# Kernel optimization log

Hardware: AMD Instinct MI355X
Metric: run time of the kernel (lower is better)

## Reference

```python
import jax, jax.numpy as jnp
import numpy as np

EPS_FREE = True  # original uses plain division by norm, no epsilon


def _gram_schmidt_batched(xf):
    """xf: [B, n_experts, dim] -> orthonormal rows per sample, [B, n_experts, dim].
    Unrolled loop over n_experts (small, fixed); fully vectorized over B."""
    n = xf.shape[1]
    v0 = xf[:, 0]
    v0 = v0 / jnp.linalg.norm(v0, axis=-1, keepdims=True)
    basis = [v0]
    for i in range(1, n):
        v = xf[:, i]
        B = jnp.stack(basis, axis=1)                      # [B, i, dim]
        coeffs = jnp.einsum('bid,bd->bi', B, v)           # projections onto basis
        v = v - jnp.einsum('bi,bid->bd', coeffs, B)
        v = v / jnp.linalg.norm(v, axis=-1, keepdims=True)
        basis.append(v)
    return jnp.stack(basis, axis=1)


def setup_inputs() -> dict:
    key = jax.random.key(0)
    n_experts, n_task, batch_size, dim = 8, 8, 1024, 512
    x = jax.random.normal(key, (n_experts, n_task, batch_size, dim), dtype=jnp.float32)
    return {"x": x}


def reference(x):
    # x: [n_experts, n_task, batch_size, dim]
    x_t = x.transpose(1, 2, 0, 3)                         # [n_task, bs, n_experts, dim]
    n_task, bs, n_experts, dim = x_t.shape
    x_flat = x_t.reshape((n_task * bs, n_experts, dim))
    orth = _gram_schmidt_batched(x_flat)
    # faithful to source: output stays in [n_task, bs, n_experts, dim] layout
    return orth.reshape((n_task, bs, n_experts, dim))
```

## Files before the change

### kernel.cpp

```cpp
#include <hip/hip_runtime.h>


#define NE 8
#define DIM 512
#define NSAMP 8192

__device__ __forceinline__ float wave_sum(float p) {
#pragma unroll
    for (int off = 32; off > 0; off >>= 1)
        p += __shfl_xor(p, off, 64);
    return p;
}

__global__ __launch_bounds__(256) void gs_kernel(const float* __restrict__ x,
                                                 float* __restrict__ out) {
    const int lane = threadIdx.x & 63;
    const int w = blockIdx.x * 4 + (threadIdx.x >> 6);
    const int t = w >> 10;
    const int b = w & 1023;

    float v[NE][8];
#pragma unroll
    for (int e = 0; e < NE; ++e) {
        const float* src = x + ((size_t)(e * 8 + t) * 1024 + b) * DIM;
#pragma unroll
        for (int c = 0; c < 2; ++c) {
            float4 f = *reinterpret_cast<const float4*>(src + c * 256 + lane * 4);
            v[e][c * 4 + 0] = f.x;
            v[e][c * 4 + 1] = f.y;
            v[e][c * 4 + 2] = f.z;
            v[e][c * 4 + 3] = f.w;
        }
    }

#pragma unroll
    for (int i = 0; i < NE; ++i) {
        float coef[NE];
#pragma unroll
        for (int j = 0; j < NE; ++j) {
            if (j < i) {
                float p = 0.f;
#pragma unroll
                for (int k = 0; k < 8; ++k) p = fmaf(v[j][k], v[i][k], p);
                coef[j] = wave_sum(p);
            }
        }
#pragma unroll
        for (int k = 0; k < 8; ++k) {
            float acc = 0.f;
#pragma unroll
            for (int j = 0; j < NE; ++j) {
                if (j < i) acc = fmaf(coef[j], v[j][k], acc);
            }
            v[i][k] -= acc;
        }
        float p = 0.f;
#pragma unroll
        for (int k = 0; k < 8; ++k) p = fmaf(v[i][k], v[i][k], p);
        float nrm2 = wave_sum(p);
        float inv = 1.0f / sqrtf(nrm2);
#pragma unroll
        for (int k = 0; k < 8; ++k) v[i][k] *= inv;
    }

#pragma unroll
    for (int e = 0; e < NE; ++e) {
        float* dst = out + ((size_t)w * NE + e) * DIM;
#pragma unroll
        for (int c = 0; c < 2; ++c) {
            float4 f;
            f.x = v[e][c * 4 + 0];
            f.y = v[e][c * 4 + 1];
            f.z = v[e][c * 4 + 2];
            f.w = v[e][c * 4 + 3];
            *reinterpret_cast<float4*>(dst + c * 256 + lane * 4) = f;
        }
    }
}

extern "C" void kernel_launch(void* const* d_in, const int* in_sizes, int n_in,
                              void* d_out, int out_size, void* d_ws, size_t ws_size,
                              hipStream_t stream) {
    const float* x = (const float*)d_in[0];
    float* out = (float*)d_out;
    gs_kernel<<<NSAMP / 4, 256, 0, stream>>>(x, out);
}
```

Measured before the change: 46.79 us.

## Replace sequential Gram-Schmidt with Gram matrix plus Cholesky orthogonalization

Computes all 36 pairwise dot products of the 8 expert vectors up front and reduces them in one batched cross-lane shuffle pass, replacing 36 serialized wave reductions. It then runs a small Cholesky factorization in registers and applies forward substitution to build the orthonormal rows. This shortens the dependency chain of the reductions but is numerically less stable than classical Gram-Schmidt, and it raises register pressure. Output stores are also switched to nontemporal stores.

Measured after the change: 49.59 us. 1.06x slower.

```diff
diff --git a/kernel.cpp b/kernel.cpp
--- a/kernel.cpp
+++ b/kernel.cpp
@@ -5,15 +5,10 @@
 #define DIM 512
 #define NSAMP 8192
 
-__device__ __forceinline__ float wave_sum(float p) {
-#pragma unroll
-    for (int off = 32; off > 0; off >>= 1)
-        p += __shfl_xor(p, off, 64);
-    return p;
-}
+typedef float f32x4 __attribute__((ext_vector_type(4)));
 
-__global__ __launch_bounds__(256) void gs_kernel(const float* __restrict__ x,
-                                                 float* __restrict__ out) {
+__global__ __launch_bounds__(256) void gs_chol_kernel(const float* __restrict__ x,
+                                                      float* __restrict__ out) {
     const int lane = threadIdx.x & 63;
     const int w = blockIdx.x * 4 + (threadIdx.x >> 6);
     const int t = w >> 10;
@@ -25,42 +20,58 @@
         const float* src = x + ((size_t)(e * 8 + t) * 1024 + b) * DIM;
 #pragma unroll
         for (int c = 0; c < 2; ++c) {
-            float4 f = *reinterpret_cast<const float4*>(src + c * 256 + lane * 4);
-            v[e][c * 4 + 0] = f.x;
-            v[e][c * 4 + 1] = f.y;
-            v[e][c * 4 + 2] = f.z;
-            v[e][c * 4 + 3] = f.w;
+            f32x4 f = *reinterpret_cast<const f32x4*>(src + c * 256 + lane * 4);
+#pragma unroll
+            for (int k = 0; k < 4; ++k) v[e][c * 4 + k] = f[k];
+        }
+    }
+
+    float g[36];
+#pragma unroll
+    for (int i = 0; i < NE; ++i) {
+#pragma unroll
+        for (int j = 0; j <= i; ++j) {
+            float p = 0.f;
+#pragma unroll
+            for (int k = 0; k < 8; ++k) p = fmaf(v[i][k], v[j][k], p);
+            g[i * (i + 1) / 2 + j] = p;
+        }
+    }
+#pragma unroll
+    for (int off = 32; off > 0; off >>= 1) {
+#pragma unroll
+        for (int m = 0; m < 36; ++m) g[m] += __shfl_xor(g[m], off, 64);
+    }
+
+    float invd[NE];
+#pragma unroll
+    for (int i = 0; i < NE; ++i) {
+#pragma unroll
+        for (int j = 0; j <= i; ++j) {
+            float s = g[i * (i + 1) / 2 + j];
+#pragma unroll
+            for (int k = 0; k < NE; ++k) {
+                if (k < j) s = fmaf(-g[i * (i + 1) / 2 + k], g[j * (j + 1) / 2 + k], s);
+            }
+            if (j == i) {
+                invd[i] = 1.0f / sqrtf(s);
+            } else {
+                g[i * (i + 1) / 2 + j] = s * invd[j];
+            }
         }
     }
 
 #pragma unroll
     for (int i = 0; i < NE; ++i) {
-        float coef[NE];
-#pragma unroll
-        for (int j = 0; j < NE; ++j) {
-            if (j < i) {
-                float p = 0.f;
-#pragma unroll
-                for (int k = 0; k < 8; ++k) p = fmaf(v[j][k], v[i][k], p);
-                coef[j] = wave_sum(p);
-            }
-        }
 #pragma unroll
         for (int k = 0; k < 8; ++k) {
-            float acc = 0.f;
+            float acc = v[i][k];
 #pragma unroll
             for (int j = 0; j < NE; ++j) {
-                if (j < i) acc = fmaf(coef[j], v[j][k], acc);
+                if (j < i) acc = fmaf(-g[i * (i + 1) / 2 + j], v[j][k], acc);
             }
-            v[i][k] -= acc;
+            v[i][k] = acc * invd[i];
         }
-        float p = 0.f;
-#pragma unroll
-        for (int k = 0; k < 8; ++k) p = fmaf(v[i][k], v[i][k], p);
-        float nrm2 = wave_sum(p);
-        float inv = 1.0f / sqrtf(nrm2);
-#pragma unroll
-        for (int k = 0; k < 8; ++k) v[i][k] *= inv;
     }
 
 #pragma unroll
@@ -68,12 +79,10 @@
         float* dst = out + ((size_t)w * NE + e) * DIM;
 #pragma unroll
         for (int c = 0; c < 2; ++c) {
-            float4 f;
-            f.x = v[e][c * 4 + 0];
-            f.y = v[e][c * 4 + 1];
-            f.z = v[e][c * 4 + 2];
-            f.w = v[e][c * 4 + 3];
-            *reinterpret_cast<float4*>(dst + c * 256 + lane * 4) = f;
+            f32x4 f;
+#pragma unroll
+            for (int k = 0; k < 4; ++k) f[k] = v[e][c * 4 + k];
+            __builtin_nontemporal_store(f, reinterpret_cast<f32x4*>(dst + c * 256 + lane * 4));
         }
     }
 }
@@ -83,5 +92,5 @@
                               hipStream_t stream) {
     const float* x = (const float*)d_in[0];
     float* out = (float*)d_out;
-    gs_kernel<<<NSAMP / 4, 256, 0, stream>>>(x, out);
+    gs_chol_kernel<<<NSAMP / 4, 256, 0, stream>>>(x, out);
 }
```
